# Kernel optimization log

Measured on AMD Instinct MI355X. Metric: run time of the kernel, lower is better.

## Reference

```python
import jax, jax.numpy as jnp
import numpy as np

QMAX = 127.0  # int8 symmetric range used by quanto absmax quantizer


def setup_inputs() -> dict:
    key = jax.random.key(0)
    k1, k2, k3 = jax.random.split(key, 3)
    x = jax.random.normal(k1, (4, 2048, 1600), dtype=jnp.float32)
    weight = jax.random.normal(k2, (1600, 6400), dtype=jnp.float32) * 0.02  # Conv1D init std=0.02
    bias = jax.random.normal(k3, (6400,), dtype=jnp.float32) * 0.02
    in_scale = jnp.float32(0.02)   # calibration scale for activations
    out_scale = jnp.float32(0.05)  # calibration scale for outputs
    return {"x": x, "weight": weight, "bias": bias, "in_scale": in_scale, "out_scale": out_scale}


def reference(x, weight, bias, in_scale, out_scale):
    # --- quantize input to int8 with the fixed in_scale (QTensor.quantize) ---
    x_q = jnp.clip(jnp.round(x / in_scale), -128, 127).astype(jnp.int32)
    # --- quantize weight to int8 with absmax scale (QTensor.quantize default) ---
    w_scale = jnp.max(jnp.abs(weight)) / QMAX
    w_q = jnp.clip(jnp.round(weight / w_scale), -128, 127).astype(jnp.int32)
    # --- quantize bias to int32 at the accumulator scale ---
    bias_scale = in_scale * w_scale
    b_q = jnp.round(bias / bias_scale).astype(jnp.int32)
    # --- int32-accumulated addmm: [B*S, nx] @ [nx, nf] + [nf] ---
    bsz = x.shape[:-1]
    nx = x.shape[-1]
    acc_i32 = jnp.matmul(x_q.reshape(-1, nx), w_q,
                         preferred_element_type=jnp.int32) + b_q[None, :]
    # --- rescale int32 accumulator (scale=bias_scale) to int8 at out_scale ---
    out_q = jnp.clip(jnp.round(acc_i32.astype(jnp.float32) * (bias_scale / out_scale)),
                     -128, 127).astype(jnp.int8)
    # return the dequantized value the downstream layer would see
    out = out_q.astype(jnp.float32) * out_scale
    return out.reshape(*bsz, -1)
```

## Files before the change

### kernel.cpp

```cpp
#include <hip/hip_runtime.h>


#define M_DIM 8192
#define K_DIM 1600
#define N_DIM 6400
#define QMAXF 127.0f

typedef __attribute__((ext_vector_type(4))) int int4v;
typedef __attribute__((ext_vector_type(16))) int int16v;


__device__ __forceinline__ void load_lds16(const void* gptr, void* lptr) {
    __builtin_amdgcn_global_load_lds((__attribute__((address_space(1))) void*)gptr,
                                     (__attribute__((address_space(3))) void*)lptr,
                                     16, 0, 0);
}

__global__ void quantx_kernel(const float* __restrict__ x, signed char* __restrict__ xq,
                              const float* __restrict__ in_scale_p,
                              unsigned int* __restrict__ wmax_bits, int n16) {
    if (blockIdx.x == 0 && threadIdx.x == 0) *wmax_bits = 0u;
    const float s = *in_scale_p;
    const float4* x4 = (const float4*)x;
    int i = blockIdx.x * blockDim.x + threadIdx.x;
    const int stride = gridDim.x * blockDim.x;
    for (; i < n16; i += stride) {
        signed char tmp[16];
#pragma unroll
        for (int j = 0; j < 4; ++j) {
            float4 v = x4[(size_t)i * 4 + j];
            tmp[j * 4 + 0] = (signed char)fminf(fmaxf(rintf(v.x / s), -128.0f), 127.0f);
            tmp[j * 4 + 1] = (signed char)fminf(fmaxf(rintf(v.y / s), -128.0f), 127.0f);
            tmp[j * 4 + 2] = (signed char)fminf(fmaxf(rintf(v.z / s), -128.0f), 127.0f);
            tmp[j * 4 + 3] = (signed char)fminf(fmaxf(rintf(v.w / s), -128.0f), 127.0f);
        }
        *(int4v*)&xq[(size_t)i * 16] = *(const int4v*)tmp;
    }
}

__global__ void wmax_kernel(const float* __restrict__ w,
                            unsigned int* __restrict__ wmax_bits, int n4) {
    __shared__ float smax[4];
    const float4* w4 = (const float4*)w;
    int i = blockIdx.x * blockDim.x + threadIdx.x;
    int stride = gridDim.x * blockDim.x;
    float m = 0.0f;
    for (; i < n4; i += stride) {
        float4 v = w4[i];
        m = fmaxf(m, fmaxf(fmaxf(fabsf(v.x), fabsf(v.y)),
                           fmaxf(fabsf(v.z), fabsf(v.w))));
    }
#pragma unroll
    for (int off = 32; off > 0; off >>= 1)
        m = fmaxf(m, __shfl_down(m, off, 64));
    const int wave = threadIdx.x >> 6;
    if ((threadIdx.x & 63) == 0) smax[wave] = m;
    __syncthreads();
    if (threadIdx.x == 0) {
        float mm = fmaxf(fmaxf(smax[0], smax[1]), fmaxf(smax[2], smax[3]));
        atomicMax(wmax_bits, __float_as_uint(mm));
    }
}

__global__ void quantw_kernel(const float* __restrict__ w, signed char* __restrict__ wT,
                              const unsigned int* __restrict__ wmax_bits) {
    __shared__ signed char tile[64 * 80];
    const float wscale = __uint_as_float(*wmax_bits) / QMAXF;
    const int n0 = blockIdx.x * 64;
    const int k0 = blockIdx.y * 64;
    const int tid = threadIdx.x;
    const int nn = tid & 63;
    const int kb = tid >> 6;
#pragma unroll
    for (int p = 0; p < 16; ++p) {
        const int kk = p * 4 + kb;
        float v = w[(size_t)(k0 + kk) * N_DIM + n0 + nn];
        float q = fminf(fmaxf(rintf(v / wscale), -128.0f), 127.0f);
        tile[nn * 80 + kk] = (signed char)q;
    }
    __syncthreads();
    const int n_loc = tid >> 2;
    const int kq = tid & 3;
    int4v val = *(const int4v*)&tile[n_loc * 80 + kq * 16];
    *(int4v*)&wT[(size_t)(n0 + n_loc) * K_DIM + k0 + kq * 16] = val;
}

__global__ __launch_bounds__(256, 3) void gemm_i8_kernel(
        const signed char* __restrict__ xq, const signed char* __restrict__ wTq,
        const float* __restrict__ bias, const unsigned int* __restrict__ wmax_bits,
        const float* __restrict__ in_scale_p, const float* __restrict__ out_scale_p,
        float* __restrict__ out) {
    __shared__ signed char A_lds[3][128 * 64];
    __shared__ signed char B_lds[3][128 * 64];

    const int tid   = threadIdx.x;
    const int wave  = tid >> 6;
    const int lane  = tid & 63;
    const int l31   = lane & 31;
    const int hi    = lane >> 5;
    const int waveM = wave >> 1;
    const int waveN = wave & 1;

    const int gid   = blockIdx.x;
    const int xcd   = gid & 7;
    const int idx   = gid >> 3;
    const int n_blk = idx >> 3;
    const int m_blk = (xcd << 3) | (idx & 7);

    const int blockN0 = n_blk * 128;
    const int blockM0 = m_blk * 128;

    const signed char* Ag = xq  + (size_t)blockM0 * K_DIM;
    const signed char* Bg = wTq + (size_t)blockN0 * K_DIM;

    const int srow = wave * 16 + (lane >> 2);
    const int sswz = (((lane >> 3) & 3) ^ ((2 * wave + (lane >> 5)) & 3));
    const int scol = (((lane & 3) ^ sswz) * 16);

    int16v acc[2][2];
#pragma unroll
    for (int mi = 0; mi < 2; ++mi)
#pragma unroll
        for (int ni = 0; ni < 2; ++ni)
#pragma unroll
            for (int r = 0; r < 16; ++r) acc[mi][ni][r] = 0;

    const int rswz = ((l31 >> 1) ^ (l31 >> 3)) & 3;

    const int NT = K_DIM / 64;

    auto STAGE = [&](int sb, int kt) {
        const int kof = kt * 64;
#pragma unroll
        for (int t = 0; t < 2; ++t) {
            const int r = t * 64 + srow;
            load_lds16(Ag + (size_t)r * K_DIM + kof + scol,
                       &A_lds[sb][(t * 64 + wave * 16) * 64]);
            load_lds16(Bg + (size_t)r * K_DIM + kof + scol,
                       &B_lds[sb][(t * 64 + wave * 16) * 64]);
        }
    };

    auto COMPUTE = [&](int cb) {
        int4v a[2][2], b[2][2];
#pragma unroll
        for (int ks = 0; ks < 2; ++ks)
#pragma unroll
            for (int ti = 0; ti < 2; ++ti) {
                const int ch = ((((ks << 1) | hi) ^ rswz) << 4);
                a[ks][ti] = *(const int4v*)
                    &A_lds[cb][(waveM * 64 + ti * 32 + l31) * 64 + ch];
                b[ks][ti] = *(const int4v*)
                    &B_lds[cb][(waveN * 64 + ti * 32 + l31) * 64 + ch];
            }
#pragma unroll
        for (int ks = 0; ks < 2; ++ks)
#pragma unroll
            for (int mi = 0; mi < 2; ++mi)
#pragma unroll
                for (int ni = 0; ni < 2; ++ni)
                    acc[mi][ni] = __builtin_amdgcn_mfma_i32_32x32x32_i8(
                        a[ks][mi], b[ks][ni], acc[mi][ni], 0, 0, 0);
    };

    STAGE(0, 0);
    STAGE(1, 1);

    int cb = 0;
    for (int t = 0; t < NT - 2; ++t) {
        const int sb = (cb == 0) ? 2 : cb - 1;
        STAGE(sb, t + 2);
        asm volatile("s_waitcnt vmcnt(8)" ::: "memory");
        __builtin_amdgcn_s_barrier();
        __builtin_amdgcn_sched_barrier(0);
        COMPUTE(cb);
        asm volatile("s_waitcnt lgkmcnt(0)" ::: "memory");
        __builtin_amdgcn_sched_barrier(0);
        __builtin_amdgcn_s_barrier();
        cb = (cb == 2) ? 0 : cb + 1;
    }

    asm volatile("s_waitcnt vmcnt(4)" ::: "memory");
    __builtin_amdgcn_s_barrier();
    __builtin_amdgcn_sched_barrier(0);
    COMPUTE(cb);
    cb = (cb == 2) ? 0 : cb + 1;

    asm volatile("s_waitcnt vmcnt(0)" ::: "memory");
    __builtin_amdgcn_s_barrier();
    __builtin_amdgcn_sched_barrier(0);
    COMPUTE(cb);

    const float s_in  = *in_scale_p;
    const float s_out = *out_scale_p;
    const float wscale = __uint_as_float(*wmax_bits) / QMAXF;
    const float bias_scale = s_in * wscale;
    const float ratio = bias_scale / s_out;

#pragma unroll
    for (int ni = 0; ni < 2; ++ni) {
        const int col = blockN0 + waveN * 64 + ni * 32 + l31;
        const int bq = (int)rintf(bias[col] / bias_scale);
#pragma unroll
        for (int mi = 0; mi < 2; ++mi) {
#pragma unroll
            for (int reg = 0; reg < 16; ++reg) {
                const int row = blockM0 + waveM * 64 + mi * 32 +
                                (reg & 3) + 8 * (reg >> 2) + 4 * hi;
                const int av = acc[mi][ni][reg] + bq;
                float f = rintf((float)av * ratio);
                f = fminf(fmaxf(f, -128.0f), 127.0f);
                __builtin_nontemporal_store(f * s_out, &out[(size_t)row * N_DIM + col]);
            }
        }
    }
}

extern "C" void kernel_launch(void* const* d_in, const int* in_sizes, int n_in,
                              void* d_out, int out_size, void* d_ws, size_t ws_size,
                              hipStream_t stream) {
    const float* x         = (const float*)d_in[0];
    const float* w         = (const float*)d_in[1];
    const float* bias      = (const float*)d_in[2];
    const float* in_scale  = (const float*)d_in[3];
    const float* out_scale = (const float*)d_in[4];
    float* out = (float*)d_out;

    unsigned char* ws = (unsigned char*)d_ws;
    unsigned int* wmax_bits = (unsigned int*)ws;
    signed char* xq  = (signed char*)(ws + 256);
    signed char* wTq = (signed char*)(ws + 256 + (size_t)M_DIM * K_DIM);

    quantx_kernel<<<2048, 256, 0, stream>>>(x, xq, in_scale, wmax_bits,
                                            M_DIM * K_DIM / 16);

    wmax_kernel<<<320, 256, 0, stream>>>(w, wmax_bits, (K_DIM * N_DIM) / 4);

    dim3 wgrid(N_DIM / 64, K_DIM / 64);
    quantw_kernel<<<wgrid, 256, 0, stream>>>(w, wTq, wmax_bits);

    gemm_i8_kernel<<<3200, 256, 0, stream>>>(xq, wTq, bias, wmax_bits,
                                             in_scale, out_scale, out);
}
```

Baseline: 384.6 us.

## Fuse quantization prep kernels into one cooperative kernel with grid sync

Merges the x quantization, weight absmax reduction and weight transpose-quantization into a single cooperative kernel. A grid-wide sync replaces the atomic max and the separate launches, with per-block partial maxima reduced after the sync. Separately, the GEMM raises wave priority around the MFMA block via s_setprio. This cuts launch gaps and a global atomic, but relies on cooperative launch with 1024 co-resident blocks and adds a grid barrier.

Result: slower. 507.4 us (+31.9%).

```diff
diff --git a/kernel.cpp b/kernel.cpp
--- a/kernel.cpp
+++ b/kernel.cpp
@@ -1,4 +1,7 @@
 #include <hip/hip_runtime.h>
+#include <hip/hip_cooperative_groups.h>
+
+namespace cg = cooperative_groups;
 
 
 #define M_DIM 8192
@@ -16,15 +19,21 @@
                                      16, 0, 0);
 }
 
-__global__ void quantx_kernel(const float* __restrict__ x, signed char* __restrict__ xq,
-                              const float* __restrict__ in_scale_p,
-                              unsigned int* __restrict__ wmax_bits, int n16) {
-    if (blockIdx.x == 0 && threadIdx.x == 0) *wmax_bits = 0u;
+__global__ __launch_bounds__(256, 4) void prep_kernel(
+        const float* __restrict__ x, signed char* __restrict__ xq,
+        const float* __restrict__ in_scale_p,
+        const float* __restrict__ w, signed char* __restrict__ wT,
+        float* __restrict__ partials, float* __restrict__ gmax_p) {
+    __shared__ signed char tile[64 * 80];
+    __shared__ float smax[4];
+
+    const int tid     = threadIdx.x;
+    const int gtid    = blockIdx.x * 256 + tid;
+    const int gstride = gridDim.x * 256;
+
     const float s = *in_scale_p;
     const float4* x4 = (const float4*)x;
-    int i = blockIdx.x * blockDim.x + threadIdx.x;
-    const int stride = gridDim.x * blockDim.x;
-    for (; i < n16; i += stride) {
+    for (int i = gtid; i < M_DIM * K_DIM / 16; i += gstride) {
         signed char tmp[16];
 #pragma unroll
         for (int j = 0; j < 4; ++j) {
@@ -36,16 +45,10 @@
         }
         *(int4v*)&xq[(size_t)i * 16] = *(const int4v*)tmp;
     }
-}
-
-__global__ void wmax_kernel(const float* __restrict__ w,
-                            unsigned int* __restrict__ wmax_bits, int n4) {
-    __shared__ float smax[4];
+
     const float4* w4 = (const float4*)w;
-    int i = blockIdx.x * blockDim.x + threadIdx.x;
-    int stride = gridDim.x * blockDim.x;
     float m = 0.0f;
-    for (; i < n4; i += stride) {
+    for (int i = gtid; i < K_DIM * N_DIM / 4; i += gstride) {
         float4 v = w4[i];
         m = fmaxf(m, fmaxf(fmaxf(fabsf(v.x), fabsf(v.y)),
                            fmaxf(fabsf(v.z), fabsf(v.w))));
@@ -53,41 +56,52 @@
 #pragma unroll
     for (int off = 32; off > 0; off >>= 1)
         m = fmaxf(m, __shfl_down(m, off, 64));
-    const int wave = threadIdx.x >> 6;
-    if ((threadIdx.x & 63) == 0) smax[wave] = m;
+    if ((tid & 63) == 0) smax[tid >> 6] = m;
     __syncthreads();
-    if (threadIdx.x == 0) {
-        float mm = fmaxf(fmaxf(smax[0], smax[1]), fmaxf(smax[2], smax[3]));
-        atomicMax(wmax_bits, __float_as_uint(mm));
-    }
-}
-
-__global__ void quantw_kernel(const float* __restrict__ w, signed char* __restrict__ wT,
-                              const unsigned int* __restrict__ wmax_bits) {
-    __shared__ signed char tile[64 * 80];
-    const float wscale = __uint_as_float(*wmax_bits) / QMAXF;
-    const int n0 = blockIdx.x * 64;
-    const int k0 = blockIdx.y * 64;
-    const int tid = threadIdx.x;
+    if (tid == 0)
+        partials[blockIdx.x] = fmaxf(fmaxf(smax[0], smax[1]),
+                                     fmaxf(smax[2], smax[3]));
+
+    cg::this_grid().sync();
+
+    float mm = 0.0f;
+    for (int j = tid; j < (int)gridDim.x; j += 256) mm = fmaxf(mm, partials[j]);
+#pragma unroll
+    for (int off = 32; off > 0; off >>= 1)
+        mm = fmaxf(mm, __shfl_down(mm, off, 64));
+    __syncthreads();
+    if ((tid & 63) == 0) smax[tid >> 6] = mm;
+    __syncthreads();
+    const float gmax = fmaxf(fmaxf(smax[0], smax[1]), fmaxf(smax[2], smax[3]));
+    if (blockIdx.x == 0 && tid == 0) *gmax_p = gmax;
+    const float wscale = gmax / QMAXF;
+
+    const int tiles_n = N_DIM / 64;
+    const int n_tiles = tiles_n * (K_DIM / 64);
     const int nn = tid & 63;
     const int kb = tid >> 6;
-#pragma unroll
-    for (int p = 0; p < 16; ++p) {
-        const int kk = p * 4 + kb;
-        float v = w[(size_t)(k0 + kk) * N_DIM + n0 + nn];
-        float q = fminf(fmaxf(rintf(v / wscale), -128.0f), 127.0f);
-        tile[nn * 80 + kk] = (signed char)q;
-    }
-    __syncthreads();
-    const int n_loc = tid >> 2;
-    const int kq = tid & 3;
-    int4v val = *(const int4v*)&tile[n_loc * 80 + kq * 16];
-    *(int4v*)&wT[(size_t)(n0 + n_loc) * K_DIM + k0 + kq * 16] = val;
+    for (int t = blockIdx.x; t < n_tiles; t += gridDim.x) {
+        const int n0 = (t % tiles_n) * 64;
+        const int k0 = (t / tiles_n) * 64;
+        __syncthreads();
+#pragma unroll
+        for (int p = 0; p < 16; ++p) {
+            const int kk = p * 4 + kb;
+            float v = w[(size_t)(k0 + kk) * N_DIM + n0 + nn];
+            float q = fminf(fmaxf(rintf(v / wscale), -128.0f), 127.0f);
+            tile[nn * 80 + kk] = (signed char)q;
+        }
+        __syncthreads();
+        const int n_loc = tid >> 2;
+        const int kq = tid & 3;
+        int4v val = *(const int4v*)&tile[n_loc * 80 + kq * 16];
+        *(int4v*)&wT[(size_t)(n0 + n_loc) * K_DIM + k0 + kq * 16] = val;
+    }
 }
 
 __global__ __launch_bounds__(256, 3) void gemm_i8_kernel(
         const signed char* __restrict__ xq, const signed char* __restrict__ wTq,
-        const float* __restrict__ bias, const unsigned int* __restrict__ wmax_bits,
+        const float* __restrict__ bias, const float* __restrict__ gmax_p,
         const float* __restrict__ in_scale_p, const float* __restrict__ out_scale_p,
         float* __restrict__ out) {
     __shared__ signed char A_lds[3][128 * 64];
@@ -153,6 +167,7 @@
                 b[ks][ti] = *(const int4v*)
                     &B_lds[cb][(waveN * 64 + ti * 32 + l31) * 64 + ch];
             }
+        __builtin_amdgcn_s_setprio(1);
 #pragma unroll
         for (int ks = 0; ks < 2; ++ks)
 #pragma unroll
@@ -161,6 +176,7 @@
                 for (int ni = 0; ni < 2; ++ni)
                     acc[mi][ni] = __builtin_amdgcn_mfma_i32_32x32x32_i8(
                         a[ks][mi], b[ks][ni], acc[mi][ni], 0, 0, 0);
+        __builtin_amdgcn_s_setprio(0);
     };
 
     STAGE(0, 0);
@@ -193,7 +209,7 @@
 
     const float s_in  = *in_scale_p;
     const float s_out = *out_scale_p;
-    const float wscale = __uint_as_float(*wmax_bits) / QMAXF;
+    const float wscale = *gmax_p / QMAXF;
     const float bias_scale = s_in * wscale;
     const float ratio = bias_scale / s_out;
 
@@ -227,18 +243,16 @@
     float* out = (float*)d_out;
 
     unsigned char* ws = (unsigned char*)d_ws;
-    unsigned int* wmax_bits = (unsigned int*)ws;
-    signed char* xq  = (signed char*)(ws + 256);
-    signed char* wTq = (signed char*)(ws + 256 + (size_t)M_DIM * K_DIM);
-
-    quantx_kernel<<<2048, 256, 0, stream>>>(x, xq, in_scale, wmax_bits,
-                                            M_DIM * K_DIM / 16);
-
-    wmax_kernel<<<320, 256, 0, stream>>>(w, wmax_bits, (K_DIM * N_DIM) / 4);
-
-    dim3 wgrid(N_DIM / 64, K_DIM / 64);
-    quantw_kernel<<<wgrid, 256, 0, stream>>>(w, wTq, wmax_bits);
-
-    gemm_i8_kernel<<<3200, 256, 0, stream>>>(xq, wTq, bias, wmax_bits,
+    float* partials = (float*)ws;
+    float* gmax_p   = (float*)(ws + 4096);
+    signed char* xq  = (signed char*)(ws + 4352);
+    signed char* wTq = xq + (size_t)M_DIM * K_DIM;
+
+    void* args[] = {(void*)&x, (void*)&xq, (void*)&in_scale, (void*)&w,
+                    (void*)&wTq, (void*)&partials, (void*)&gmax_p};
+    hipLaunchCooperativeKernel((const void*)prep_kernel, dim3(1024), dim3(256),
+                               args, 0, stream);
+
+    gemm_i8_kernel<<<3200, 256, 0, stream>>>(xq, wTq, bias, gmax_p,
                                              in_scale, out_scale, out);
 }
```
